# Performance work log

Measured on AMD Instinct MI355X. Metric: run time of the kernel, lower is better.

## Reference

```python
import jax, jax.numpy as jnp
import numpy as np

D_MODEL = 1024
N_HEADS = 16
WINDOW = 256
CAUSAL = True


def build_sliding_window_mask(T, window_size, causal=True):
    half = window_size // 2
    i = jnp.arange(T)[:, None]
    j = jnp.arange(T)[None, :]
    attend = jnp.abs(i - j) <= half
    if causal:
        attend = attend & (j <= i)
    return jnp.where(attend, 0.0, -jnp.inf).astype(jnp.float32)  # (T, T)


def setup_inputs() -> dict:
    key = jax.random.key(0)
    kx, kq, kk, kv, ko = jax.random.split(key, 5)
    B, T, D = 2, 2048, D_MODEL
    s = 1.0 / np.sqrt(D)
    return {
        "x": jax.random.normal(kx, (B, T, D), jnp.float32),
        "Wq": jax.random.normal(kq, (D, D), jnp.float32) * s,
        "Wk": jax.random.normal(kk, (D, D), jnp.float32) * s,
        "Wv": jax.random.normal(kv, (D, D), jnp.float32) * s,
        "Wo": jax.random.normal(ko, (D, D), jnp.float32) * s,
    }


def reference(x, Wq, Wk, Wv, Wo):
    B, T, D = x.shape
    H = N_HEADS
    dh = D // H
    # torch nn.Linear: y = x @ W.T
    def proj(W):
        return (x @ W.T).reshape(B, T, H, dh).transpose(0, 2, 1, 3)  # (B,H,T,dh)

    q, k, v = proj(Wq), proj(Wk), proj(Wv)
    scale = jnp.sqrt(jnp.asarray(dh, x.dtype))
    scores = jnp.einsum("bhtd,bhsd->bhts", q, k) / scale  # (B,H,T,T)
    mask = build_sliding_window_mask(T, WINDOW, CAUSAL)
    scores = scores + mask[None, None]
    attn = jax.nn.softmax(scores, axis=-1)
    attn = jnp.nan_to_num(attn, nan=0.0)
    out = jnp.einsum("bhts,bhsd->bhtd", attn, v)  # (B,H,T,dh)
    out = out.transpose(0, 2, 1, 3).reshape(B, T, D)
    return out @ Wo.T
```

## Files before the change

### kernel.cpp

```cpp
#include <hip/hip_runtime.h>
#include <hip/hip_bf16.h>

#define B_  2
#define T_  2048
#define D_  1024
#define H_  16
#define DH_ 64
#define M_  (B_ * T_)

typedef short s16x8 __attribute__((ext_vector_type(8)));
typedef float f32x4 __attribute__((ext_vector_type(4)));

__device__ inline float bfu(unsigned short u) {
    union { unsigned int i; float f; } c; c.i = ((unsigned int)u) << 16; return c.f;
}
__device__ inline unsigned short f2bf(float f) {
    union { float f; unsigned int i; } c; c.f = f;
    unsigned int r = c.i + 0x7fffu + ((c.i >> 16) & 1u);
    return (unsigned short)(r >> 16);
}
__device__ inline void stv(float* p, float v) { *p = v; }
__device__ inline void stv(unsigned short* p, float v) { *p = f2bf(v); }

__device__ inline void gload_lds16(const unsigned short* g, unsigned short* l) {
    __builtin_amdgcn_global_load_lds(
        (const __attribute__((address_space(1))) void*)g,
        (__attribute__((address_space(3))) void*)l, 16, 0, 0);
}

__global__ __launch_bounds__(256) void conv_bf16(const float* __restrict__ x,
                                                 const float* __restrict__ Wq,
                                                 const float* __restrict__ Wk,
                                                 const float* __restrict__ Wv,
                                                 const float* __restrict__ Wo,
                                                 unsigned short* __restrict__ dst) {
    const int g = blockIdx.x * 256 + threadIdx.x;
    const float* s; size_t o;
    if (g < (1 << 20)) { s = x; o = (size_t)g; }
    else {
        int gg = g - (1 << 20);
        int w = gg >> 18;
        o = (size_t)(gg & ((1 << 18) - 1));
        s = (w == 0) ? Wq : (w == 1) ? Wk : (w == 2) ? Wv : Wo;
    }
    float4 v = ((const float4*)s)[o];
    ushort4 u;
    u.x = f2bf(v.x); u.y = f2bf(v.y); u.z = f2bf(v.z); u.w = f2bf(v.w);
    ((ushort4*)dst)[g] = u;
}

template <int BM, int BN, int NH, typename Tout>
__global__ __launch_bounds__(256) void gemm_m97(const unsigned short* __restrict__ A,
                                                const unsigned short* __restrict__ Bw,
                                                Tout* __restrict__ C0,
                                                Tout* __restrict__ C1,
                                                unsigned short* __restrict__ vtr,
                                                int K) {
    constexpr int MI = BM / 32;
    constexpr int NI = BN / 32;
    __shared__ unsigned short As[NH * BM * 32];
    __shared__ unsigned short Bs[NH * BN * 32];
    const int tid  = threadIdx.x;
    const int lane = tid & 63;
    const int wave = tid >> 6;
    const int wr = wave >> 1, wc = wave & 1;
    const int bm = blockIdx.y * BM, bn = blockIdx.x * BN;
    const int fr = lane & 15, kg = lane >> 4;
    const int lrow = lane >> 2;
    const int lcol = (lane & 3) * 8;

    f32x4 acc[MI][NI];
    #pragma unroll
    for (int mi = 0; mi < MI; ++mi)
        #pragma unroll
        for (int ni = 0; ni < NI; ++ni)
            #pragma unroll
            for (int r = 0; r < 4; ++r) acc[mi][ni][r] = 0.f;

    const unsigned short* ga = A  + (size_t)(bm + wave * 16 + lrow) * K + lcol;
    const unsigned short* gb = Bw + (size_t)(bn + wave * 16 + lrow) * K + lcol;
    unsigned short* la = &As[(wave * 16) * 32];
    unsigned short* lb = &Bs[(wave * 16) * 32];

    for (int k0 = 0; k0 < K; k0 += 32 * NH) {
        __syncthreads();
        #pragma unroll
        for (int hf = 0; hf < NH; ++hf) {
            #pragma unroll
            for (int s = 0; s < BM / 64; ++s)
                gload_lds16(ga + k0 + hf * 32 + (size_t)(s * 64) * K,
                            la + hf * BM * 32 + s * 64 * 32);
            #pragma unroll
            for (int s = 0; s < BN / 64; ++s)
                gload_lds16(gb + k0 + hf * 32 + (size_t)(s * 64) * K,
                            lb + hf * BN * 32 + s * 64 * 32);
        }
        __syncthreads();
        #pragma unroll
        for (int hf = 0; hf < NH; ++hf) {
            s16x8 af[MI], bfv[NI];
            #pragma unroll
            for (int mi = 0; mi < MI; ++mi)
                af[mi] = *(const s16x8*)&As[hf * BM * 32 + (wr * (BM / 2) + mi * 16 + fr) * 32 + kg * 8];
            #pragma unroll
            for (int ni = 0; ni < NI; ++ni)
                bfv[ni] = *(const s16x8*)&Bs[hf * BN * 32 + (wc * (BN / 2) + ni * 16 + fr) * 32 + kg * 8];
            #pragma unroll
            for (int mi = 0; mi < MI; ++mi)
                #pragma unroll
                for (int ni = 0; ni < NI; ++ni)
                    acc[mi][ni] = __builtin_amdgcn_mfma_f32_16x16x32_bf16(af[mi], bfv[ni], acc[mi][ni], 0, 0, 0);
        }
    }

    if (vtr && bn >= 2048) {
        #pragma unroll
        for (int mi = 0; mi < MI; ++mi)
            #pragma unroll
            for (int ni = 0; ni < NI; ++ni) {
                const int nl = (bn - 2048) + wc * (BN / 2) + ni * 16 + fr;
                const int h = nl >> 6, d = nl & 63;
                const int m0 = bm + wr * (BM / 2) + mi * 16 + kg * 4;
                const int b = m0 >> 11, t0 = m0 & (T_ - 1);
                ushort4 u;
                u.x = f2bf(acc[mi][ni][0]); u.y = f2bf(acc[mi][ni][1]);
                u.z = f2bf(acc[mi][ni][2]); u.w = f2bf(acc[mi][ni][3]);
                *(ushort4*)(vtr + ((size_t)(b * H_ + h) * 64 + d) * T_ + t0) = u;
            }
        return;
    }
    Tout* C = (bn < 1024) ? C0 : C1;
    const int nb = bn & 1023;
    #pragma unroll
    for (int mi = 0; mi < MI; ++mi)
        #pragma unroll
        for (int ni = 0; ni < NI; ++ni)
            #pragma unroll
            for (int r = 0; r < 4; ++r) {
                int m = bm + wr * (BM / 2) + mi * 16 + kg * 4 + r;
                int n = nb + wc * (BN / 2) + ni * 16 + fr;
                stv(&C[(size_t)m * 1024 + n], acc[mi][ni][r]);
            }
}

__global__ __launch_bounds__(256) void swa_mfma4(const unsigned short* qb,
                                                 const unsigned short* __restrict__ kb,
                                                 const unsigned short* __restrict__ vt,
                                                 unsigned short* ob) {
    __shared__ unsigned short Ks[192 * 64];
    __shared__ unsigned short Vs[64 * 208];
    const int wave = threadIdx.x >> 6;
    const int lane = threadIdx.x & 63;
    const int blk = blockIdx.x;
    const int i0b = (blk & 31) * 64;
    const int bh  = blk >> 5;
    const int h = bh & (H_ - 1), b = bh >> 4;
    const int g = lane >> 4, l15 = lane & 15;

    const size_t rowbase = (size_t)b * T_ * D_ + (size_t)h * DH_;
    const int klo2 = (i0b > 128) ? (i0b - 128) : 0;

    {
        const int lr = lane >> 3;
        const int gc = (lane & 7) ^ lr;
        const unsigned short* kg0 = kb + rowbase + (size_t)(klo2 + lr) * D_ + gc * 8;
        #pragma unroll
        for (int s = 0; s < 6; ++s) {
            const int i = wave * 6 + s;
            gload_lds16(kg0 + (size_t)(i * 8) * D_, &Ks[i * 8 * 64]);
        }
    }
    {
        const unsigned short* vtb = vt + (size_t)bh * 64 * T_ + klo2;
        #pragma unroll
        for (int s = 0; s < 7; ++s) {
            const int i = s * 4 + wave;
            if (i < 26) {
                const int cc = i * 64 + lane;
                const int d  = cc / 26;
                const int sl = cc - d * 26;
                const int c  = (sl < 24) ? (sl ^ (d & 7)) : sl;
                gload_lds16(vtb + (size_t)d * T_ + c * 8, &Vs[i * 512]);
            }
        }
    }

    const int i0  = i0b + wave * 16;
    const int klo = (i0 > 128) ? (i0 - 128) : 0;
    const int koff = klo - klo2;

    const unsigned short* qrow = qb + rowbase + (size_t)(i0 + l15) * D_ + g * 8;
    const s16x8 aq0 = *(const s16x8*)(qrow);
    const s16x8 aq1 = *(const s16x8*)(qrow + 32);

    __syncthreads();

    f32x4 sacc[9];
    #pragma unroll
    for (int t = 0; t < 9; ++t)
        #pragma unroll
        for (int r = 0; r < 4; ++r) sacc[t][r] = 0.f;

    #pragma unroll
    for (int t = 0; t < 9; ++t) {
        const int row = koff + t * 16 + l15;
        const int r7 = row & 7;
        s16x8 b0 = *(const s16x8*)&Ks[row * 64 + ((g     ^ r7) * 8)];
        s16x8 b1 = *(const s16x8*)&Ks[row * 64 + (((g+4) ^ r7) * 8)];
        sacc[t] = __builtin_amdgcn_mfma_f32_16x16x32_bf16(aq0, b0, sacc[t], 0, 0, 0);
        sacc[t] = __builtin_amdgcn_mfma_f32_16x16x32_bf16(aq1, b1, sacc[t], 0, 0, 0);
    }

    __syncthreads();
    unsigned short* Pw = &Ks[wave * (16 * 168)];
    {
        int row = lane >> 2, col = 144 + (lane & 3) * 4;
        *(uint2*)&Pw[row * 168 + col] = make_uint2(0u, 0u);
    }

    float mrow[4] = {-1e30f, -1e30f, -1e30f, -1e30f};
    #pragma unroll
    for (int t = 0; t < 9; ++t)
        #pragma unroll
        for (int r = 0; r < 4; ++r) {
            const int j  = klo + t * 16 + l15;
            const int iq = i0 + g * 4 + r;
            const bool valid = (j <= iq) && (j + 128 >= iq);
            const float s = valid ? sacc[t][r] * 0.125f : -1e30f;
            sacc[t][r] = s;
            mrow[r] = fmaxf(mrow[r], s);
        }
    #pragma unroll
    for (int r = 0; r < 4; ++r)
        #pragma unroll
        for (int off = 1; off < 16; off <<= 1)
            mrow[r] = fmaxf(mrow[r], __shfl_xor(mrow[r], off));

    float lrow[4] = {0.f, 0.f, 0.f, 0.f};
    #pragma unroll
    for (int t = 0; t < 9; ++t)
        #pragma unroll
        for (int r = 0; r < 4; ++r) {
            const float p = __expf(sacc[t][r] - mrow[r]);
            sacc[t][r] = p;
            lrow[r] += p;
        }
    #pragma unroll
    for (int r = 0; r < 4; ++r) {
        #pragma unroll
        for (int off = 1; off < 16; off <<= 1)
            lrow[r] += __shfl_xor(lrow[r], off);
    }
    float invl[4];
    #pragma unroll
    for (int r = 0; r < 4; ++r) invl[r] = 1.f / lrow[r];

    #pragma unroll
    for (int t = 0; t < 9; ++t)
        #pragma unroll
        for (int r = 0; r < 4; ++r)
            Pw[(g * 4 + r) * 168 + t * 16 + l15] = f2bf(sacc[t][r]);

    f32x4 oacc[4];
    #pragma unroll
    for (int nt = 0; nt < 4; ++nt)
        #pragma unroll
        for (int r = 0; r < 4; ++r) oacc[nt][r] = 0.f;

    const int kc0 = koff >> 3;
    #pragma unroll
    for (int kt = 0; kt < 5; ++kt) {
        const s16x8 ap = *(const s16x8*)&Pw[l15 * 168 + kt * 32 + g * 8];
        #pragma unroll
        for (int nt = 0; nt < 4; ++nt) {
            const int d = nt * 16 + l15;
            const int c = kc0 + kt * 4 + g;
            const int sl = (c < 24) ? (c ^ (d & 7)) : c;
            s16x8 bv = *(const s16x8*)&Vs[d * 208 + sl * 8];
            oacc[nt] = __builtin_amdgcn_mfma_f32_16x16x32_bf16(ap, bv, oacc[nt], 0, 0, 0);
        }
    }

    #pragma unroll
    for (int nt = 0; nt < 4; ++nt)
        #pragma unroll
        for (int r = 0; r < 4; ++r) {
            const float val = oacc[nt][r] * invl[r];
            ob[rowbase + (size_t)(i0 + g * 4 + r) * D_ + nt * 16 + l15] = f2bf(val);
        }
}

extern "C" void kernel_launch(void* const* d_in, const int* in_sizes, int n_in,
                              void* d_out, int out_size, void* d_ws, size_t ws_size,
                              hipStream_t stream) {
    const float* x  = (const float*)d_in[0];
    const float* Wq = (const float*)d_in[1];
    const float* Wk = (const float*)d_in[2];
    const float* Wv = (const float*)d_in[3];
    const float* Wo = (const float*)d_in[4];

    const size_t MD = (size_t)M_ * D_;
    const size_t WN = (size_t)D_ * D_;

    unsigned short* wsb = (unsigned short*)d_ws;
    unsigned short* xb  = wsb;
    unsigned short* Wqb = xb + MD;
    unsigned short* Wob = Wqb + 3 * WN;
    unsigned short* qb  = Wob + WN;
    unsigned short* vt = (unsigned short*)d_out;
    unsigned short* kb = vt + MD;

    conv_bf16<<<8192, 256, 0, stream>>>(x, Wq, Wk, Wv, Wo, wsb);

    gemm_m97<128, 128, 2, unsigned short><<<dim3(24, M_ / 128), 256, 0, stream>>>(
        xb, Wqb, qb, kb, vt, D_);

    swa_mfma4<<<(B_ * H_ * T_) / 64, 256, 0, stream>>>(qb, kb, vt, qb);

    gemm_m97<64, 128, 4, float><<<dim3(8, M_ / 64), 256, 0, stream>>>(
        qb, Wob, (float*)d_out, (float*)d_out, nullptr, D_);
}
```

Baseline: 149.0 us.

## Replace QKV projection GEMM with 256x256-tile, 8-wave phased pipelined kernel

Adds a new bf16 GEMM for the fused QKV projection. It uses 256x256 tiles, 512 threads, and double-buffered LDS with XOR swizzling. Each K-step is split into four MFMA quarters, with global-to-LDS loads interleaved between them, barriers in between, and s_setprio raised around the MFMA bursts. The goal is better data reuse and more overlap of memory and matrix work than the 128x128 kernel it replaces. In exchange it uses far more LDS (128KB) and registers, and the grid is only 12x16=192 blocks, which may underfill the GPU.

After: 152.6 us. 1.02x slower.

```diff
diff --git a/kernel.cpp b/kernel.cpp
--- a/kernel.cpp
+++ b/kernel.cpp
@@ -143,6 +143,180 @@
             }
 }
 
+template <int K>
+__global__ __launch_bounds__(512) void gemm_8ph(const unsigned short* __restrict__ A,
+                                                const unsigned short* __restrict__ Bw,
+                                                unsigned short* __restrict__ C0,
+                                                unsigned short* __restrict__ C1,
+                                                unsigned short* __restrict__ vtr) {
+    constexpr int NKT = K / 64;
+    static_assert(NKT >= 4 && (NKT & 1) == 0, "peel assumes even NKT>=4");
+    __shared__ unsigned short As[2][256 * 64];
+    __shared__ unsigned short Bs[2][256 * 64];
+    const int tid  = threadIdx.x;
+    const int lane = tid & 63;
+    const int w    = tid >> 6;
+    const int wm = w >> 2, wn = w & 3;
+    const int fr = lane & 15, kg = lane >> 4, fr7 = lane & 7;
+    const int bm = blockIdx.y * 256, bn = blockIdx.x * 256;
+
+    const int srow = lane >> 3;
+    const int schk = (lane & 7) ^ srow;
+    const unsigned short* ga = A  + (size_t)(bm + w * 8 + srow) * K + schk * 8;
+    const unsigned short* gb = Bw + (size_t)(bn + w * 8 + srow) * K + schk * 8;
+    unsigned short* lA0 = &As[0][(w * 8) * 64];
+    unsigned short* lB0 = &Bs[0][(w * 8) * 64];
+
+    f32x4 acc[8][4];
+    #pragma unroll
+    for (int i = 0; i < 8; ++i)
+        #pragma unroll
+        for (int j = 0; j < 4; ++j)
+            #pragma unroll
+            for (int r = 0; r < 4; ++r) acc[i][j][r] = 0.f;
+
+    s16x8 av[4][2], bv[4][2];
+
+#define STG_A(q, t, h)                                                         \
+    gload_lds16(ga + (size_t)((h) * 128) * K + (size_t)(t) * 64,               \
+                lA0 + ((q) * 256 + (h) * 128) * 64);                           \
+    gload_lds16(ga + (size_t)((h) * 128 + 64) * K + (size_t)(t) * 64,          \
+                lA0 + ((q) * 256 + (h) * 128 + 64) * 64)
+#define STG_B(q, t, h)                                                         \
+    gload_lds16(gb + (size_t)((h) * 128) * K + (size_t)(t) * 64,               \
+                lB0 + ((q) * 256 + (h) * 128) * 64);                           \
+    gload_lds16(gb + (size_t)((h) * 128 + 64) * K + (size_t)(t) * 64,          \
+                lB0 + ((q) * 256 + (h) * 128 + 64) * 64)
+#define LDA(mh, q)                                                             \
+    _Pragma("unroll")                                                          \
+    for (int i = 0; i < 4; ++i) {                                              \
+        const int row = wm * 128 + ((mh) * 4 + i) * 16 + fr;                   \
+        av[i][0] = *(const s16x8*)&As[(q)][row * 64 + ((kg ^ fr7) * 8)];       \
+        av[i][1] = *(const s16x8*)&As[(q)][row * 64 + (((4 + kg) ^ fr7) * 8)]; \
+    }
+#define LDB(q)                                                                 \
+    _Pragma("unroll")                                                          \
+    for (int i = 0; i < 4; ++i) {                                              \
+        const int row = wn * 64 + i * 16 + fr;                                 \
+        bv[i][0] = *(const s16x8*)&Bs[(q)][row * 64 + ((kg ^ fr7) * 8)];       \
+        bv[i][1] = *(const s16x8*)&Bs[(q)][row * 64 + (((4 + kg) ^ fr7) * 8)]; \
+    }
+#define MFMAQ(mh, nh)                                                          \
+    __builtin_amdgcn_s_setprio(1);                                             \
+    _Pragma("unroll")                                                          \
+    for (int i = 0; i < 4; ++i)                                                \
+        _Pragma("unroll")                                                      \
+        for (int j = 0; j < 2; ++j) {                                          \
+            acc[(mh) * 4 + i][(nh) * 2 + j] =                                  \
+                __builtin_amdgcn_mfma_f32_16x16x32_bf16(                       \
+                    av[i][0], bv[(nh) * 2 + j][0],                             \
+                    acc[(mh) * 4 + i][(nh) * 2 + j], 0, 0, 0);                 \
+            acc[(mh) * 4 + i][(nh) * 2 + j] =                                  \
+                __builtin_amdgcn_mfma_f32_16x16x32_bf16(                       \
+                    av[i][1], bv[(nh) * 2 + j][1],                             \
+                    acc[(mh) * 4 + i][(nh) * 2 + j], 0, 0, 0);                 \
+        }                                                                      \
+    __builtin_amdgcn_s_setprio(0)
+#define BAR()   __builtin_amdgcn_s_barrier()
+#define LGKM0() asm volatile("s_waitcnt lgkmcnt(0)" ::: "memory")
+#define VMW(n)  asm volatile("s_waitcnt vmcnt(" #n ")" ::: "memory")
+
+    STG_A(0, 0, 0); STG_A(0, 0, 1);
+    STG_B(0, 0, 0); STG_B(0, 0, 1);
+    STG_B(1, 1, 0); STG_B(1, 1, 1);
+    VMW(4);
+    BAR();
+
+    #pragma unroll 2
+    for (int d = 0; d < NKT - 2; ++d) {
+        const int q = d & 1;
+        LDA(0, q); LDB(q);
+        STG_A(q ^ 1, d + 1, 0);
+        BAR(); LGKM0();
+        MFMAQ(0, 0);
+        BAR();
+        STG_A(q ^ 1, d + 1, 1);
+        BAR();
+        MFMAQ(0, 1);
+        BAR();
+        LDA(1, q);
+        STG_B(q, d + 2, 0);
+        BAR(); LGKM0();
+        MFMAQ(1, 0);
+        BAR();
+        STG_B(q, d + 2, 1);
+        BAR();
+        MFMAQ(1, 1);
+        VMW(4);
+        BAR();
+    }
+    {
+        LDA(0, 0); LDB(0);
+        STG_A(1, NKT - 1, 0);
+        BAR(); LGKM0();
+        MFMAQ(0, 0);
+        BAR();
+        STG_A(1, NKT - 1, 1);
+        BAR();
+        MFMAQ(0, 1);
+        BAR();
+        LDA(1, 0);
+        BAR(); LGKM0();
+        MFMAQ(1, 0);
+        BAR();
+        MFMAQ(1, 1);
+        VMW(0);
+        BAR();
+    }
+    {
+        LDA(0, 1); LDB(1);
+        LGKM0();
+        MFMAQ(0, 0);
+        MFMAQ(0, 1);
+        LDA(1, 1);
+        LGKM0();
+        MFMAQ(1, 0);
+        MFMAQ(1, 1);
+    }
+#undef STG_A
+#undef STG_B
+#undef LDA
+#undef LDB
+#undef MFMAQ
+#undef BAR
+#undef LGKM0
+#undef VMW
+
+    if (vtr && bn >= 2048) {
+        #pragma unroll
+        for (int mf = 0; mf < 8; ++mf)
+            #pragma unroll
+            for (int nf = 0; nf < 4; ++nf) {
+                const int nl = (bn - 2048) + wn * 64 + nf * 16 + fr;
+                const int h = nl >> 6, d = nl & 63;
+                const int m0 = bm + wm * 128 + mf * 16 + kg * 4;
+                const int b = m0 >> 11, t0 = m0 & (T_ - 1);
+                ushort4 u;
+                u.x = f2bf(acc[mf][nf][0]); u.y = f2bf(acc[mf][nf][1]);
+                u.z = f2bf(acc[mf][nf][2]); u.w = f2bf(acc[mf][nf][3]);
+                *(ushort4*)(vtr + ((size_t)(b * H_ + h) * 64 + d) * T_ + t0) = u;
+            }
+        return;
+    }
+    unsigned short* C = (bn < 1024) ? C0 : C1;
+    const int nb = bn & 1023;
+    #pragma unroll
+    for (int mf = 0; mf < 8; ++mf)
+        #pragma unroll
+        for (int nf = 0; nf < 4; ++nf)
+            #pragma unroll
+            for (int r = 0; r < 4; ++r) {
+                int m = bm + wm * 128 + mf * 16 + kg * 4 + r;
+                int n = nb + wn * 64 + nf * 16 + fr;
+                C[(size_t)m * 1024 + n] = f2bf(acc[mf][nf][r]);
+            }
+}
+
 __global__ __launch_bounds__(256) void swa_mfma4(const unsigned short* qb,
                                                  const unsigned short* __restrict__ kb,
                                                  const unsigned short* __restrict__ vt,
@@ -312,8 +486,7 @@
 
     conv_bf16<<<8192, 256, 0, stream>>>(x, Wq, Wk, Wv, Wo, wsb);
 
-    gemm_m97<128, 128, 2, unsigned short><<<dim3(24, M_ / 128), 256, 0, stream>>>(
-        xb, Wqb, qb, kb, vt, D_);
+    gemm_8ph<D_><<<dim3(12, M_ / 256), 512, 0, stream>>>(xb, Wqb, qb, kb, vt);
 
     swa_mfma4<<<(B_ * H_ * T_) / 64, 256, 0, stream>>>(qb, kb, vt, qb);
 
```
